# Performance work log

Measured on AMD Instinct MI355X. Metric: run time of the kernel, lower is better.

The kernel has to match this reference:

```python
import jax, jax.numpy as jnp
import numpy as np

B, S, N, M = 64, 512, 512, 128   # batch, sensory_size, state_size, motor_size
UNFOLDS = 6
DT = 0.1  # elapsed_time


def _gate(v, mu, sigma):
    # piecewise-linear 'sigmoid': clip((v - mu + sigma) / (2 sigma), 0, 1)
    # v: [B, P] -> [B, P, 1] broadcast against [P, N]
    return jnp.clip((v[..., None] - mu + sigma) / (2.0 * sigma), 0.0, 1.0)


def setup_inputs() -> dict:
    key = jax.random.key(0)
    ks = jax.random.split(key, 12)
    u = lambda k, sh, lo, hi: jax.random.uniform(k, sh, jnp.float32, lo, hi)
    inputs = jax.random.normal(ks[0], (B, S), dtype=jnp.float32)
    states = jax.random.normal(ks[1], (B, N), dtype=jnp.float32) * 0.1
    # parameters per _init_ranges
    tau = u(ks[2], (N,), 0.001, 2.0)
    b = u(ks[3], (N,), -0.2, 0.2)
    erev = jnp.where(jax.random.bernoulli(ks[4], 0.8, (N, N)), 1.0, -1.0).astype(jnp.float32)
    w = u(ks[5], (N, N), 0.001, 1.0)
    sigma = jnp.full((N, N), 0.5, jnp.float32)
    mu = jnp.full((N, N), 0.5, jnp.float32)
    sensory_erev = jnp.where(jax.random.bernoulli(ks[6], 0.8, (S, N)), 1.0, -1.0).astype(jnp.float32)
    sensory_w = u(ks[7], (S, N), 0.001, 1.0)
    sensory_sigma = jnp.full((S, N), 0.5, jnp.float32)
    sensory_mu = jnp.full((S, N), 0.5, jnp.float32)
    sparsity_mask = jax.random.bernoulli(ks[8], 0.3, (N, N)).astype(jnp.float32)
    sensory_sparsity_mask = jax.random.bernoulli(ks[9], 0.3, (S, N)).astype(jnp.float32)
    input_w = jnp.ones((S,), jnp.float32)
    input_b = jnp.zeros((S,), jnp.float32)
    output_w = jnp.ones((M,), jnp.float32)
    output_b = jnp.zeros((M,), jnp.float32)
    return dict(inputs=inputs, states=states, tau=tau, b=b, erev=erev, w=w,
                sigma=sigma, mu=mu, sensory_erev=sensory_erev, sensory_w=sensory_w,
                sensory_sigma=sensory_sigma, sensory_mu=sensory_mu,
                sparsity_mask=sparsity_mask, sensory_sparsity_mask=sensory_sparsity_mask,
                input_w=input_w, input_b=input_b, output_w=output_w, output_b=output_b)


def reference(inputs, states, tau, b, erev, w, sigma, mu,
              sensory_erev, sensory_w, sensory_sigma, sensory_mu,
              sparsity_mask, sensory_sparsity_mask,
              input_w, input_b, output_w, output_b):
    # input mapping (affine)
    x = inputs * input_w + input_b                                   # [B, S]
    # sensory synapses, computed once
    sa = _gate(x, sensory_mu, sensory_sigma) * sensory_sparsity_mask  # [B, S, N]
    s_rev = jnp.einsum('bsn,sn->bn', sa, sensory_erev)               # [B, N]
    s_w = jnp.einsum('bsn,sn->bn', sa, sensory_w)                    # [B, N]
    delta = DT / UNFOLDS

    def step(v, _):
        g = _gate(v, mu, sigma) * sparsity_mask                      # [B, N, N]
        sum_rev = jnp.einsum('bij,ij->bj', g, erev) + s_rev + b      # sum over presynaptic i
        sum_w = jnp.einsum('bij,ij->bj', g, w) + s_w
        k = 1.0 / (1.0 + sum_w)
        taun = tau * k
        q = taun / (taun + delta)
        v_new = q * v + (1.0 - q) * k * sum_rev
        return v_new, None

    v, _ = jax.lax.scan(step, states, None, length=UNFOLDS)
    # output mapping: slice last M neurons (M < N), then affine
    out = v[:, -M:] * output_w + output_b                            # [B, M]
    return out, v
```

## Files before the change

### kernel.cpp

```cpp
#include <hip/hip_runtime.h>

constexpr int cB = 64, cS = 512, cN = 512, cM = 128;
constexpr float cDELTA = 0.016666666666666666f;

constexpr int KB = 4;
constexpr int JT = 32;
constexpr int NJT = cN / JT;
constexpr int IC = 16;
constexpr int ILEN = cN / IC;
constexpr int NT = JT * IC;
constexpr int NB = (cB / KB) * NJT;

__device__ __forceinline__ float clamp01(float x) {
    return __builtin_amdgcn_fmed3f(x, 0.0f, 1.0f);
}

template <bool USE_P>
__global__ __launch_bounds__(NT)
void k_init(const float* __restrict__ inputs, const float* __restrict__ states,
            const float* __restrict__ bias,
            const float* __restrict__ erev,  const float* __restrict__ wgt,
            const float* __restrict__ sigma, const float* __restrict__ mu,
            const float* __restrict__ serev, const float* __restrict__ swgt,
            const float* __restrict__ ssigma,const float* __restrict__ smu,
            const float* __restrict__ mask,  const float* __restrict__ smask,
            const float* __restrict__ inw,   const float* __restrict__ inb,
            float4* __restrict__ P, float* __restrict__ srb,
            float* __restrict__ swS, float* __restrict__ vA)
{
    const int tid = threadIdx.x, bid = blockIdx.x;
    const int bg = bid >> 4, jt = bid & (NJT - 1);
    const int b0 = bg * KB, j0 = jt * JT;
    const int jl = tid & (JT - 1), ic = tid >> 5;
    const int j = j0 + jl;

    __shared__ float xsh[cS * KB];
    __shared__ float redR[KB * IC * JT];
    __shared__ float redW[KB * IC * JT];

    if constexpr (USE_P) {
        for (int idx = bid * NT + tid; idx < cN * cN; idx += NB * NT) {
            float sg = sigma[idx];
            float a  = 0.5f / sg;
            float c  = fmaf(-mu[idx], a, 0.5f);
            float mk = mask[idx];
            P[idx] = make_float4(a, c, erev[idx] * mk, wgt[idx] * mk);
        }
    }

    for (int t = tid; t < cS * KB; t += NT) {
        int bb = t >> 9, s = t & (cS - 1);
        xsh[s * KB + bb] = fmaf(inputs[(b0 + bb) * cS + s], inw[s], inb[s]);
    }
    __syncthreads();

    float aR[KB] = {0.f, 0.f, 0.f, 0.f}, aW[KB] = {0.f, 0.f, 0.f, 0.f};
    int idx = (ic * ILEN) * cN + j;
#pragma unroll 8
    for (int ii = 0; ii < ILEN; ++ii, idx += cN) {
        int s    = ic * ILEN + ii;
        float sg = ssigma[idx];
        float a  = 0.5f / sg;
        float c  = fmaf(-smu[idx], a, 0.5f);
        float mk = smask[idx];
        float e  = serev[idx] * mk;
        float wv = swgt[idx] * mk;
        const float4 xv = *(const float4*)&xsh[s * KB];
        float g;
        g = clamp01(fmaf(xv.x, a, c)); aR[0] = fmaf(g, e, aR[0]); aW[0] = fmaf(g, wv, aW[0]);
        g = clamp01(fmaf(xv.y, a, c)); aR[1] = fmaf(g, e, aR[1]); aW[1] = fmaf(g, wv, aW[1]);
        g = clamp01(fmaf(xv.z, a, c)); aR[2] = fmaf(g, e, aR[2]); aW[2] = fmaf(g, wv, aW[2]);
        g = clamp01(fmaf(xv.w, a, c)); aR[3] = fmaf(g, e, aR[3]); aW[3] = fmaf(g, wv, aW[3]);
    }
#pragma unroll
    for (int b = 0; b < KB; ++b) {
        redR[(b * IC + ic) * JT + jl] = aR[b];
        redW[(b * IC + ic) * JT + jl] = aW[b];
    }
    __syncthreads();

    if (tid < JT * KB) {
        int jj = tid & (JT - 1), bb = tid >> 5;
        float r = 0.f, wv = 0.f;
#pragma unroll
        for (int c2 = 0; c2 < IC; ++c2) {
            r  += redR[(bb * IC + c2) * JT + jj];
            wv += redW[(bb * IC + c2) * JT + jj];
        }
        int jg   = j0 + jj;
        int gidx = (b0 + bb) * cN + jg;
        srb[gidx] = r + bias[jg];
        swS[gidx] = wv;
        vA[gidx]  = states[gidx];
    }
}

template <bool USE_P, bool LAST>
__global__ __launch_bounds__(NT)
void k_unfold(const float* __restrict__ vin, float* __restrict__ vout,
              const float4* __restrict__ P,
              const float* __restrict__ erev,  const float* __restrict__ wgt,
              const float* __restrict__ sigma, const float* __restrict__ mu,
              const float* __restrict__ mask,
              const float* __restrict__ srb,   const float* __restrict__ swS,
              const float* __restrict__ tau,
              const float* __restrict__ outw,  const float* __restrict__ outb,
              float* __restrict__ out)
{
    const int tid = threadIdx.x, bid = blockIdx.x;
    const int bg = bid >> 4, jt = bid & (NJT - 1);
    const int b0 = bg * KB, j0 = jt * JT;
    const int jl = tid & (JT - 1), ic = tid >> 5;
    const int j = j0 + jl;

    __shared__ float vsh[cN * KB];
    __shared__ float redR[KB * IC * JT];
    __shared__ float redW[KB * IC * JT];

    float my_srb = 0.f, my_sw = 0.f, my_tau = 0.f, my_ow = 0.f, my_ob = 0.f;
    int my_gidx = 0, my_jg = 0, my_mi = -1;
    if (tid < JT * KB) {
        int jj = tid & (JT - 1), bb = tid >> 5;
        my_jg   = j0 + jj;
        my_gidx = (b0 + bb) * cN + my_jg;
        my_srb  = srb[my_gidx];
        my_sw   = swS[my_gidx];
        my_tau  = tau[my_jg];
        if (LAST && my_jg >= cN - cM) {
            int m = my_jg - (cN - cM);
            my_ow = outw[m];
            my_ob = outb[m];
            my_mi = (b0 + bb) * cM + m;
        }
    }

    for (int t = tid; t < cN * KB; t += NT) {
        int bb = t >> 9, i = t & (cN - 1);
        vsh[i * KB + bb] = vin[(b0 + bb) * cN + i];
    }
    __syncthreads();

    float aR[KB] = {0.f, 0.f, 0.f, 0.f}, aW[KB] = {0.f, 0.f, 0.f, 0.f};
    int idx = (ic * ILEN) * cN + j;
    int vo  = (ic * ILEN) * KB;
#pragma unroll 8
    for (int ii = 0; ii < ILEN; ++ii, idx += cN, vo += KB) {
        float a, c, e, wv;
        if constexpr (USE_P) {
            float4 p = P[idx];
            a = p.x; c = p.y; e = p.z; wv = p.w;
        } else {
            float sg = sigma[idx];
            a  = 0.5f / sg;
            c  = fmaf(-mu[idx], a, 0.5f);
            float mk = mask[idx];
            e  = erev[idx] * mk;
            wv = wgt[idx]  * mk;
        }
        const float4 vv = *(const float4*)&vsh[vo];
        float g;
        g = clamp01(fmaf(vv.x, a, c)); aR[0] = fmaf(g, e, aR[0]); aW[0] = fmaf(g, wv, aW[0]);
        g = clamp01(fmaf(vv.y, a, c)); aR[1] = fmaf(g, e, aR[1]); aW[1] = fmaf(g, wv, aW[1]);
        g = clamp01(fmaf(vv.z, a, c)); aR[2] = fmaf(g, e, aR[2]); aW[2] = fmaf(g, wv, aW[2]);
        g = clamp01(fmaf(vv.w, a, c)); aR[3] = fmaf(g, e, aR[3]); aW[3] = fmaf(g, wv, aW[3]);
    }
#pragma unroll
    for (int b = 0; b < KB; ++b) {
        redR[(b * IC + ic) * JT + jl] = aR[b];
        redW[(b * IC + ic) * JT + jl] = aW[b];
    }
    __syncthreads();

    if (tid < JT * KB) {
        int jj = tid & (JT - 1), bb = tid >> 5;
        float r = 0.f, wv = 0.f;
#pragma unroll
        for (int c2 = 0; c2 < IC; ++c2) {
            r  += redR[(bb * IC + c2) * JT + jj];
            wv += redW[(bb * IC + c2) * JT + jj];
        }
        r  += my_srb;
        wv += my_sw;
        float k    = 1.0f / (1.0f + wv);
        float taun = my_tau * k;
        float inv  = 1.0f / (taun + cDELTA);
        float vold = vsh[my_jg * KB + bb];
        float vn   = (taun * inv) * vold + (cDELTA * inv) * k * r;
        vout[my_gidx] = vn;
        if (LAST && my_mi >= 0) out[my_mi] = fmaf(vn, my_ow, my_ob);
    }
}

extern "C" void kernel_launch(void* const* d_in, const int* in_sizes, int n_in,
                              void* d_out, int out_size, void* d_ws, size_t ws_size,
                              hipStream_t stream)
{
    const float* inputs = (const float*)d_in[0];
    const float* states = (const float*)d_in[1];
    const float* tau    = (const float*)d_in[2];
    const float* bias   = (const float*)d_in[3];
    const float* erev   = (const float*)d_in[4];
    const float* wgt    = (const float*)d_in[5];
    const float* sigma  = (const float*)d_in[6];
    const float* mu     = (const float*)d_in[7];
    const float* serev  = (const float*)d_in[8];
    const float* swgt   = (const float*)d_in[9];
    const float* ssigma = (const float*)d_in[10];
    const float* smu    = (const float*)d_in[11];
    const float* mask   = (const float*)d_in[12];
    const float* smask  = (const float*)d_in[13];
    const float* inw    = (const float*)d_in[14];
    const float* inb    = (const float*)d_in[15];
    const float* outw   = (const float*)d_in[16];
    const float* outb   = (const float*)d_in[17];
    float* out = (float*)d_out;
    float* ws  = (float*)d_ws;

    const size_t pfloats = (size_t)cN * cN * 4;
    const bool use_p = ws_size >= (pfloats + 3ull * cB * cN) * sizeof(float);

    float4* P; float* srb; float* swS; float* vB;
    if (use_p) {
        P   = (float4*)ws;
        srb = ws + pfloats;
    } else {
        P   = nullptr;
        srb = ws;
    }
    swS = srb + cB * cN;
    vB  = swS + cB * cN;
    float* vA = out + cB * cM;

    if (use_p) {
        k_init<true><<<NB, NT, 0, stream>>>(inputs, states, bias, erev, wgt, sigma, mu,
                                            serev, swgt, ssigma, smu, mask, smask,
                                            inw, inb, P, srb, swS, vA);
        k_unfold<true, false><<<NB, NT, 0, stream>>>(vA, vB, P, erev, wgt, sigma, mu, mask,
                                                     srb, swS, tau, outw, outb, out);
        k_unfold<true, false><<<NB, NT, 0, stream>>>(vB, vA, P, erev, wgt, sigma, mu, mask,
                                                     srb, swS, tau, outw, outb, out);
        k_unfold<true, false><<<NB, NT, 0, stream>>>(vA, vB, P, erev, wgt, sigma, mu, mask,
                                                     srb, swS, tau, outw, outb, out);
        k_unfold<true, false><<<NB, NT, 0, stream>>>(vB, vA, P, erev, wgt, sigma, mu, mask,
                                                     srb, swS, tau, outw, outb, out);
        k_unfold<true, false><<<NB, NT, 0, stream>>>(vA, vB, P, erev, wgt, sigma, mu, mask,
                                                     srb, swS, tau, outw, outb, out);
        k_unfold<true, true ><<<NB, NT, 0, stream>>>(vB, vA, P, erev, wgt, sigma, mu, mask,
                                                     srb, swS, tau, outw, outb, out);
    } else {
        k_init<false><<<NB, NT, 0, stream>>>(inputs, states, bias, erev, wgt, sigma, mu,
                                             serev, swgt, ssigma, smu, mask, smask,
                                             inw, inb, P, srb, swS, vA);
        k_unfold<false, false><<<NB, NT, 0, stream>>>(vA, vB, P, erev, wgt, sigma, mu, mask,
                                                      srb, swS, tau, outw, outb, out);
        k_unfold<false, false><<<NB, NT, 0, stream>>>(vB, vA, P, erev, wgt, sigma, mu, mask,
                                                      srb, swS, tau, outw, outb, out);
        k_unfold<false, false><<<NB, NT, 0, stream>>>(vA, vB, P, erev, wgt, sigma, mu, mask,
                                                      srb, swS, tau, outw, outb, out);
        k_unfold<false, false><<<NB, NT, 0, stream>>>(vB, vA, P, erev, wgt, sigma, mu, mask,
                                                      srb, swS, tau, outw, outb, out);
        k_unfold<false, false><<<NB, NT, 0, stream>>>(vA, vB, P, erev, wgt, sigma, mu, mask,
                                                      srb, swS, tau, outw, outb, out);
        k_unfold<false, true ><<<NB, NT, 0, stream>>>(vB, vA, P, erev, wgt, sigma, mu, mask,
                                                      srb, swS, tau, outw, outb, out);
    }
}
```

Before: 137.1 us.

## Fuse unfolds into one cooperative persistent kernel with grid barrier and mu/sigma fast path

Replaces six separate unfold launches with one cooperative kernel that loops over unfolds and uses an atomic counter grid barrier between steps. It also detects at runtime whether mu=0.5 and sigma=0.5 everywhere (a=1, c=0). When that holds, it precomputes the clamped state once per element and streams only a float2 of erev/w instead of a float4. It also doubles the reduction chunk count to 1024 threads per block and drops the workspace-size fallback. The gains target launch overhead and memory traffic, at the cost of spin-barrier latency and a hard requirement that all blocks be co-resident.

```diff
diff --git a/kernel.cpp b/kernel.cpp
--- a/kernel.cpp
+++ b/kernel.cpp
@@ -1,33 +1,44 @@
 #include <hip/hip_runtime.h>
 
-constexpr int cB = 64, cS = 512, cN = 512, cM = 128;
+constexpr int cB = 64, cS = 512, cN = 512, cM = 128, cUNF = 6;
 constexpr float cDELTA = 0.016666666666666666f;
 
 constexpr int KB = 4;
 constexpr int JT = 32;
 constexpr int NJT = cN / JT;
-constexpr int IC = 16;
+constexpr int IC = 32;
 constexpr int ILEN = cN / IC;
 constexpr int NT = JT * IC;
 constexpr int NB = (cB / KB) * NJT;
 
+constexpr size_t OFF_P4  = 0;
+constexpr size_t OFF_EW  = (size_t)cN * cN * 4;
+constexpr size_t OFF_SRB = OFF_EW + (size_t)cN * cN * 2;
+constexpr size_t OFF_SW  = OFF_SRB + (size_t)cB * cN;
+constexpr size_t OFF_VA  = OFF_SW  + (size_t)cB * cN;
+constexpr size_t OFF_VB  = OFF_VA  + (size_t)cB * cN;
+constexpr size_t OFF_CTR = OFF_VB  + (size_t)cB * cN;
+
 __device__ __forceinline__ float clamp01(float x) {
     return __builtin_amdgcn_fmed3f(x, 0.0f, 1.0f);
 }
 
-template <bool USE_P>
 __global__ __launch_bounds__(NT)
-void k_init(const float* __restrict__ inputs, const float* __restrict__ states,
-            const float* __restrict__ bias,
+void k_init(const float* __restrict__ inputs, const float* __restrict__ bias,
             const float* __restrict__ erev,  const float* __restrict__ wgt,
             const float* __restrict__ sigma, const float* __restrict__ mu,
             const float* __restrict__ serev, const float* __restrict__ swgt,
             const float* __restrict__ ssigma,const float* __restrict__ smu,
             const float* __restrict__ mask,  const float* __restrict__ smask,
             const float* __restrict__ inw,   const float* __restrict__ inb,
-            float4* __restrict__ P, float* __restrict__ srb,
-            float* __restrict__ swS, float* __restrict__ vA)
+            float* __restrict__ ws)
 {
+    float4* P4 = (float4*)(ws + OFF_P4);
+    float2* EW = (float2*)(ws + OFF_EW);
+    float* srb = ws + OFF_SRB;
+    float* swS = ws + OFF_SW;
+    int*   ctr = (int*)(ws + OFF_CTR);
+
     const int tid = threadIdx.x, bid = blockIdx.x;
     const int bg = bid >> 4, jt = bid & (NJT - 1);
     const int b0 = bg * KB, j0 = jt * JT;
@@ -38,34 +49,42 @@
     __shared__ float redR[KB * IC * JT];
     __shared__ float redW[KB * IC * JT];
 
-    if constexpr (USE_P) {
-        for (int idx = bid * NT + tid; idx < cN * cN; idx += NB * NT) {
-            float sg = sigma[idx];
-            float a  = 0.5f / sg;
-            float c  = fmaf(-mu[idx], a, 0.5f);
-            float mk = mask[idx];
-            P[idx] = make_float4(a, c, erev[idx] * mk, wgt[idx] * mk);
-        }
-    }
-
-    for (int t = tid; t < cS * KB; t += NT) {
-        int bb = t >> 9, s = t & (cS - 1);
-        xsh[s * KB + bb] = fmaf(inputs[(b0 + bb) * cS + s], inw[s], inb[s]);
+    {
+        int idx  = bid * NT + tid;
+        float sg = sigma[idx];
+        float a  = 0.5f / sg;
+        float c  = fmaf(-mu[idx], a, 0.5f);
+        float mk = mask[idx];
+        float e  = erev[idx] * mk;
+        float w  = wgt[idx]  * mk;
+        P4[idx] = make_float4(a, c, e, w);
+        EW[idx] = make_float2(e, w);
+        int ok = (a == 1.0f) && (c == 0.0f);
+        if (!__syncthreads_and(ok)) {
+            if (tid == 0) atomicAdd(&ctr[8], 1);
+        }
+    }
+
+#pragma unroll
+    for (int r = 0; r < (cS * KB) / NT; ++r) {
+        int t = tid + r * NT;
+        int bb = t & 3, s = t >> 2;
+        xsh[t] = fmaf(inputs[(b0 + bb) * cS + s], inw[s], inb[s]);
     }
     __syncthreads();
 
     float aR[KB] = {0.f, 0.f, 0.f, 0.f}, aW[KB] = {0.f, 0.f, 0.f, 0.f};
     int idx = (ic * ILEN) * cN + j;
-#pragma unroll 8
-    for (int ii = 0; ii < ILEN; ++ii, idx += cN) {
-        int s    = ic * ILEN + ii;
+    int xo  = (ic * ILEN) * KB;
+#pragma unroll 4
+    for (int ii = 0; ii < ILEN; ++ii, idx += cN, xo += KB) {
         float sg = ssigma[idx];
         float a  = 0.5f / sg;
         float c  = fmaf(-smu[idx], a, 0.5f);
         float mk = smask[idx];
         float e  = serev[idx] * mk;
         float wv = swgt[idx] * mk;
-        const float4 xv = *(const float4*)&xsh[s * KB];
+        const float4 xv = *(const float4*)&xsh[xo];
         float g;
         g = clamp01(fmaf(xv.x, a, c)); aR[0] = fmaf(g, e, aR[0]); aW[0] = fmaf(g, wv, aW[0]);
         g = clamp01(fmaf(xv.y, a, c)); aR[1] = fmaf(g, e, aR[1]); aW[1] = fmaf(g, wv, aW[1]);
@@ -87,26 +106,26 @@
             r  += redR[(bb * IC + c2) * JT + jj];
             wv += redW[(bb * IC + c2) * JT + jj];
         }
-        int jg   = j0 + jj;
+        int jg = j0 + jj;
         int gidx = (b0 + bb) * cN + jg;
         srb[gidx] = r + bias[jg];
         swS[gidx] = wv;
-        vA[gidx]  = states[gidx];
-    }
-}
-
-template <bool USE_P, bool LAST>
+    }
+}
+
 __global__ __launch_bounds__(NT)
-void k_unfold(const float* __restrict__ vin, float* __restrict__ vout,
-              const float4* __restrict__ P,
-              const float* __restrict__ erev,  const float* __restrict__ wgt,
-              const float* __restrict__ sigma, const float* __restrict__ mu,
-              const float* __restrict__ mask,
-              const float* __restrict__ srb,   const float* __restrict__ swS,
-              const float* __restrict__ tau,
-              const float* __restrict__ outw,  const float* __restrict__ outb,
-              float* __restrict__ out)
+void k_unfolds(const float* __restrict__ states, const float* __restrict__ tau,
+               const float* __restrict__ outw,   const float* __restrict__ outb,
+               float* __restrict__ out, float* __restrict__ ws)
 {
+    const float4* P4 = (const float4*)(ws + OFF_P4);
+    const float2* EW = (const float2*)(ws + OFF_EW);
+    const float* srb = ws + OFF_SRB;
+    const float* swS = ws + OFF_SW;
+    float* vA = ws + OFF_VA;
+    float* vB = ws + OFF_VB;
+    int*   ctr = (int*)(ws + OFF_CTR);
+
     const int tid = threadIdx.x, bid = blockIdx.x;
     const int bg = bid >> 4, jt = bid & (NJT - 1);
     const int b0 = bg * KB, j0 = jt * JT;
@@ -118,76 +137,103 @@
     __shared__ float redW[KB * IC * JT];
 
     float my_srb = 0.f, my_sw = 0.f, my_tau = 0.f, my_ow = 0.f, my_ob = 0.f;
-    int my_gidx = 0, my_jg = 0, my_mi = -1;
+    int my_gidx = 0, my_mi = -1;
     if (tid < JT * KB) {
         int jj = tid & (JT - 1), bb = tid >> 5;
-        my_jg   = j0 + jj;
-        my_gidx = (b0 + bb) * cN + my_jg;
+        int jg = j0 + jj;
+        my_gidx = (b0 + bb) * cN + jg;
         my_srb  = srb[my_gidx];
         my_sw   = swS[my_gidx];
-        my_tau  = tau[my_jg];
-        if (LAST && my_jg >= cN - cM) {
-            int m = my_jg - (cN - cM);
-            my_ow = outw[m];
-            my_ob = outb[m];
+        my_tau  = tau[jg];
+        if (jg >= cN - cM) {
+            int m = jg - (cN - cM);
+            my_ow = outw[m]; my_ob = outb[m];
             my_mi = (b0 + bb) * cM + m;
         }
     }
-
-    for (int t = tid; t < cN * KB; t += NT) {
-        int bb = t >> 9, i = t & (cN - 1);
-        vsh[i * KB + bb] = vin[(b0 + bb) * cN + i];
-    }
-    __syncthreads();
-
-    float aR[KB] = {0.f, 0.f, 0.f, 0.f}, aW[KB] = {0.f, 0.f, 0.f, 0.f};
-    int idx = (ic * ILEN) * cN + j;
-    int vo  = (ic * ILEN) * KB;
+    const int fast = (ctr[8] == 0);
+
+    const float* vin = states;
+    for (int u = 0; u < cUNF; ++u) {
+        float* vout = (u == cUNF - 1) ? (out + cB * cM) : ((u & 1) ? vA : vB);
+
+#pragma unroll
+        for (int r = 0; r < (cN * KB) / NT; ++r) {
+            int t = tid + r * NT;
+            int bb = t & 3, ii = t >> 2;
+            float vv = __hip_atomic_load(&vin[(b0 + bb) * cN + ii],
+                                         __ATOMIC_RELAXED, __HIP_MEMORY_SCOPE_AGENT);
+            vsh[t] = fast ? clamp01(vv) : vv;
+        }
+        __syncthreads();
+
+        float aR[KB] = {0.f, 0.f, 0.f, 0.f}, aW[KB] = {0.f, 0.f, 0.f, 0.f};
+        int idx = (ic * ILEN) * cN + j;
+        int vo  = (ic * ILEN) * KB;
+        if (fast) {
 #pragma unroll 8
-    for (int ii = 0; ii < ILEN; ++ii, idx += cN, vo += KB) {
-        float a, c, e, wv;
-        if constexpr (USE_P) {
-            float4 p = P[idx];
-            a = p.x; c = p.y; e = p.z; wv = p.w;
+            for (int ii = 0; ii < ILEN; ++ii, idx += cN, vo += KB) {
+                const float2 ew = EW[idx];
+                const float4 g4 = *(const float4*)&vsh[vo];
+                aR[0] = fmaf(g4.x, ew.x, aR[0]); aW[0] = fmaf(g4.x, ew.y, aW[0]);
+                aR[1] = fmaf(g4.y, ew.x, aR[1]); aW[1] = fmaf(g4.y, ew.y, aW[1]);
+                aR[2] = fmaf(g4.z, ew.x, aR[2]); aW[2] = fmaf(g4.z, ew.y, aW[2]);
+                aR[3] = fmaf(g4.w, ew.x, aR[3]); aW[3] = fmaf(g4.w, ew.y, aW[3]);
+            }
         } else {
-            float sg = sigma[idx];
-            a  = 0.5f / sg;
-            c  = fmaf(-mu[idx], a, 0.5f);
-            float mk = mask[idx];
-            e  = erev[idx] * mk;
-            wv = wgt[idx]  * mk;
-        }
-        const float4 vv = *(const float4*)&vsh[vo];
-        float g;
-        g = clamp01(fmaf(vv.x, a, c)); aR[0] = fmaf(g, e, aR[0]); aW[0] = fmaf(g, wv, aW[0]);
-        g = clamp01(fmaf(vv.y, a, c)); aR[1] = fmaf(g, e, aR[1]); aW[1] = fmaf(g, wv, aW[1]);
-        g = clamp01(fmaf(vv.z, a, c)); aR[2] = fmaf(g, e, aR[2]); aW[2] = fmaf(g, wv, aW[2]);
-        g = clamp01(fmaf(vv.w, a, c)); aR[3] = fmaf(g, e, aR[3]); aW[3] = fmaf(g, wv, aW[3]);
-    }
-#pragma unroll
-    for (int b = 0; b < KB; ++b) {
-        redR[(b * IC + ic) * JT + jl] = aR[b];
-        redW[(b * IC + ic) * JT + jl] = aW[b];
-    }
-    __syncthreads();
-
-    if (tid < JT * KB) {
-        int jj = tid & (JT - 1), bb = tid >> 5;
-        float r = 0.f, wv = 0.f;
-#pragma unroll
-        for (int c2 = 0; c2 < IC; ++c2) {
-            r  += redR[(bb * IC + c2) * JT + jj];
-            wv += redW[(bb * IC + c2) * JT + jj];
-        }
-        r  += my_srb;
-        wv += my_sw;
-        float k    = 1.0f / (1.0f + wv);
-        float taun = my_tau * k;
-        float inv  = 1.0f / (taun + cDELTA);
-        float vold = vsh[my_jg * KB + bb];
-        float vn   = (taun * inv) * vold + (cDELTA * inv) * k * r;
-        vout[my_gidx] = vn;
-        if (LAST && my_mi >= 0) out[my_mi] = fmaf(vn, my_ow, my_ob);
+#pragma unroll 4
+            for (int ii = 0; ii < ILEN; ++ii, idx += cN, vo += KB) {
+                const float4 p  = P4[idx];
+                const float4 vv = *(const float4*)&vsh[vo];
+                float g;
+                g = clamp01(fmaf(vv.x, p.x, p.y)); aR[0] = fmaf(g, p.z, aR[0]); aW[0] = fmaf(g, p.w, aW[0]);
+                g = clamp01(fmaf(vv.y, p.x, p.y)); aR[1] = fmaf(g, p.z, aR[1]); aW[1] = fmaf(g, p.w, aW[1]);
+                g = clamp01(fmaf(vv.z, p.x, p.y)); aR[2] = fmaf(g, p.z, aR[2]); aW[2] = fmaf(g, p.w, aW[2]);
+                g = clamp01(fmaf(vv.w, p.x, p.y)); aR[3] = fmaf(g, p.z, aR[3]); aW[3] = fmaf(g, p.w, aW[3]);
+            }
+        }
+#pragma unroll
+        for (int b = 0; b < KB; ++b) {
+            redR[(b * IC + ic) * JT + jl] = aR[b];
+            redW[(b * IC + ic) * JT + jl] = aW[b];
+        }
+        __syncthreads();
+
+        if (tid < JT * KB) {
+            int jj = tid & (JT - 1), bb = tid >> 5;
+            float r = 0.f, wv = 0.f;
+#pragma unroll
+            for (int c2 = 0; c2 < IC; ++c2) {
+                r  += redR[(bb * IC + c2) * JT + jj];
+                wv += redW[(bb * IC + c2) * JT + jj];
+            }
+            r  += my_srb;
+            wv += my_sw;
+            float k    = 1.0f / (1.0f + wv);
+            float taun = my_tau * k;
+            float inv  = 1.0f / (taun + cDELTA);
+            float vold = __hip_atomic_load(&vin[my_gidx],
+                                           __ATOMIC_RELAXED, __HIP_MEMORY_SCOPE_AGENT);
+            float vn = (taun * inv) * vold + (cDELTA * inv) * k * r;
+            if (u == cUNF - 1) {
+                vout[my_gidx] = vn;
+                if (my_mi >= 0) out[my_mi] = fmaf(vn, my_ow, my_ob);
+            } else {
+                __hip_atomic_store(&vout[my_gidx], vn,
+                                   __ATOMIC_RELAXED, __HIP_MEMORY_SCOPE_AGENT);
+            }
+        }
+
+        if (u < cUNF - 1) {
+            __syncthreads();
+            if (tid == 0) {
+                __hip_atomic_fetch_add(&ctr[u], 1, __ATOMIC_RELEASE, __HIP_MEMORY_SCOPE_AGENT);
+                while (__hip_atomic_load(&ctr[u], __ATOMIC_RELAXED, __HIP_MEMORY_SCOPE_AGENT) < NB)
+                    __builtin_amdgcn_s_sleep(2);
+            }
+            __syncthreads();
+            vin = (u & 1) ? vA : vB;
+        }
     }
 }
 
@@ -216,52 +262,15 @@
     float* out = (float*)d_out;
     float* ws  = (float*)d_ws;
 
-    const size_t pfloats = (size_t)cN * cN * 4;
-    const bool use_p = ws_size >= (pfloats + 3ull * cB * cN) * sizeof(float);
-
-    float4* P; float* srb; float* swS; float* vB;
-    if (use_p) {
-        P   = (float4*)ws;
-        srb = ws + pfloats;
-    } else {
-        P   = nullptr;
-        srb = ws;
-    }
-    swS = srb + cB * cN;
-    vB  = swS + cB * cN;
-    float* vA = out + cB * cM;
-
-    if (use_p) {
-        k_init<true><<<NB, NT, 0, stream>>>(inputs, states, bias, erev, wgt, sigma, mu,
-                                            serev, swgt, ssigma, smu, mask, smask,
-                                            inw, inb, P, srb, swS, vA);
-        k_unfold<true, false><<<NB, NT, 0, stream>>>(vA, vB, P, erev, wgt, sigma, mu, mask,
-                                                     srb, swS, tau, outw, outb, out);
-        k_unfold<true, false><<<NB, NT, 0, stream>>>(vB, vA, P, erev, wgt, sigma, mu, mask,
-                                                     srb, swS, tau, outw, outb, out);
-        k_unfold<true, false><<<NB, NT, 0, stream>>>(vA, vB, P, erev, wgt, sigma, mu, mask,
-                                                     srb, swS, tau, outw, outb, out);
-        k_unfold<true, false><<<NB, NT, 0, stream>>>(vB, vA, P, erev, wgt, sigma, mu, mask,
-                                                     srb, swS, tau, outw, outb, out);
-        k_unfold<true, false><<<NB, NT, 0, stream>>>(vA, vB, P, erev, wgt, sigma, mu, mask,
-                                                     srb, swS, tau, outw, outb, out);
-        k_unfold<true, true ><<<NB, NT, 0, stream>>>(vB, vA, P, erev, wgt, sigma, mu, mask,
-                                                     srb, swS, tau, outw, outb, out);
-    } else {
-        k_init<false><<<NB, NT, 0, stream>>>(inputs, states, bias, erev, wgt, sigma, mu,
-                                             serev, swgt, ssigma, smu, mask, smask,
-                                             inw, inb, P, srb, swS, vA);
-        k_unfold<false, false><<<NB, NT, 0, stream>>>(vA, vB, P, erev, wgt, sigma, mu, mask,
-                                                      srb, swS, tau, outw, outb, out);
-        k_unfold<false, false><<<NB, NT, 0, stream>>>(vB, vA, P, erev, wgt, sigma, mu, mask,
-                                                      srb, swS, tau, outw, outb, out);
-        k_unfold<false, false><<<NB, NT, 0, stream>>>(vA, vB, P, erev, wgt, sigma, mu, mask,
-                                                      srb, swS, tau, outw, outb, out);
-        k_unfold<false, false><<<NB, NT, 0, stream>>>(vB, vA, P, erev, wgt, sigma, mu, mask,
-                                                      srb, swS, tau, outw, outb, out);
-        k_unfold<false, false><<<NB, NT, 0, stream>>>(vA, vB, P, erev, wgt, sigma, mu, mask,
-                                                      srb, swS, tau, outw, outb, out);
-        k_unfold<false, true ><<<NB, NT, 0, stream>>>(vB, vA, P, erev, wgt, sigma, mu, mask,
-                                                      srb, swS, tau, outw, outb, out);
-    }
-}
+    int* ctr = (int*)(ws + OFF_CTR);
+    hipMemsetAsync(ctr, 0, 16 * sizeof(int), stream);
+
+    k_init<<<NB, NT, 0, stream>>>(inputs, bias, erev, wgt, sigma, mu,
+                                  serev, swgt, ssigma, smu, mask, smask,
+                                  inw, inb, ws);
+
+    void* args[] = {(void*)&states, (void*)&tau, (void*)&outw, (void*)&outb,
+                    (void*)&out, (void*)&ws};
+    hipLaunchCooperativeKernel((const void*)k_unfolds, dim3(NB), dim3(NT),
+                               args, 0, stream);
+}
```

New measurement: 207.7 us. +51.4%, slower.
